# Performance work log

Hardware: AMD Instinct MI355X
Metric: run time of the kernel (lower is better)

Reference implementation:

```python
import jax, jax.numpy as jnp
import numpy as np

N, E = 100000, 1200000
IN_DIM, HID, OUT = 128, 64, 64
EPS = 1e-5


def _glorot(key, shape):
    lim = 1.0 / np.sqrt(shape[0])
    return jax.random.uniform(key, shape, jnp.float32, -lim, lim)


def setup_inputs() -> dict:
    key = jax.random.key(0)
    ks = jax.random.split(key, 20)
    inp = {
        'x': jax.random.normal(ks[0], (N, IN_DIM), jnp.float32),
        'edge_index': jax.random.randint(ks[1], (2, E), 0, N, jnp.int64),
        'xgb_scores': jax.random.uniform(ks[2], (N,), jnp.float32),
        # SAGEConv params: W_l (aggregated path, with bias), W_r (root path, no bias)
        'W1l': _glorot(ks[3], (IN_DIM, HID)), 'b1': jnp.zeros((HID,), jnp.float32), 'W1r': _glorot(ks[4], (IN_DIM, HID)),
        'g1': jnp.ones((HID,), jnp.float32), 'be1': jnp.zeros((HID,), jnp.float32),
        'W2l': _glorot(ks[5], (HID, HID)), 'b2': jnp.zeros((HID,), jnp.float32), 'W2r': _glorot(ks[6], (HID, HID)),
        'g2': jnp.ones((HID,), jnp.float32), 'be2': jnp.zeros((HID,), jnp.float32),
        'W3l': _glorot(ks[7], (HID, OUT)), 'b3': jnp.zeros((OUT,), jnp.float32), 'W3r': _glorot(ks[8], (HID, OUT)),
        'g3': jnp.ones((OUT,), jnp.float32), 'be3': jnp.zeros((OUT,), jnp.float32),
        # fusion MLP: Linear(out+1, 64) -> ReLU -> Linear(64, 1)
        'Wf1': _glorot(ks[9], (OUT + 1, 64)), 'bf1': jnp.zeros((64,), jnp.float32),
        'Wf2': _glorot(ks[10], (64, 1)), 'bf2': jnp.zeros((1,), jnp.float32),
    }
    return inp


def _sage_conv(x, src, dst, Wl, b, Wr, n):
    # mean aggregation of source features at destination nodes (PyG SAGEConv, aggr='mean')
    agg = jax.ops.segment_sum(x[src], dst, num_segments=n)           # (N, d)
    cnt = jax.ops.segment_sum(jnp.ones((src.shape[0],), x.dtype), dst, num_segments=n)
    mean = agg / jnp.clip(cnt, 1.0)[:, None]
    return mean @ Wl + b + x @ Wr


def _bn(h, g, b):
    mu = jnp.mean(h, axis=0)
    var = jnp.var(h, axis=0)  # biased, as in torch BN training normalization
    return (h - mu) * jax.lax.rsqrt(var + EPS) * g + b


def reference(x, edge_index, xgb_scores,
              W1l, b1, W1r, g1, be1,
              W2l, b2, W2r, g2, be2,
              W3l, b3, W3r, g3, be3,
              Wf1, bf1, Wf2, bf2):
    n = x.shape[0]
    src, dst = edge_index[0], edge_index[1]
    # dropout is identity in eval; BN uses batch statistics
    h = jax.nn.relu(_bn(_sage_conv(x, src, dst, W1l, b1, W1r, n), g1, be1))
    h = jax.nn.relu(_bn(_sage_conv(h, src, dst, W2l, b2, W2r, n), g2, be2))
    h = jax.nn.relu(_bn(_sage_conv(h, src, dst, W3l, b3, W3r, n), g3, be3))
    combined = jnp.concatenate([h, xgb_scores[:, None]], axis=1)     # (N, out+1)
    z = jax.nn.relu(combined @ Wf1 + bf1)
    logits = (z @ Wf2 + bf2)[:, 0]
    return logits
```

## Files before the change

### kernel.cpp

```cpp
#include <hip/hip_runtime.h>


typedef __attribute__((ext_vector_type(8))) short bf16x8;
typedef __attribute__((ext_vector_type(4))) float f32x4;

#define ELLS 48

__device__ __forceinline__ ushort f2bf(float f) {
  unsigned u = __float_as_uint(f);
  return (ushort)((u + 0x7fff + ((u >> 16) & 1)) >> 16);
}
__device__ __forceinline__ float bf2f(ushort h) {
  return __uint_as_float((unsigned)h << 16);
}
__device__ __forceinline__ void unpack8(uint4 v, float* f) {
  f[0] = __uint_as_float(v.x << 16);
  f[1] = __uint_as_float(v.x & 0xffff0000u);
  f[2] = __uint_as_float(v.y << 16);
  f[3] = __uint_as_float(v.y & 0xffff0000u);
  f[4] = __uint_as_float(v.z << 16);
  f[5] = __uint_as_float(v.z & 0xffff0000u);
  f[6] = __uint_as_float(v.w << 16);
  f[7] = __uint_as_float(v.w & 0xffff0000u);
}


__device__ __forceinline__ void prep_one(const float* __restrict__ Wl,
                                         const float* __restrict__ Wr,
                                         ushort* __restrict__ Whi,
                                         ushort* __restrict__ Wlo, int din,
                                         int i) {
  int col = i / din, k = i % din;
  float v = (col < 64) ? Wl[(size_t)k * 64 + col]
                       : Wr[(size_t)k * 64 + (col - 64)];
  ushort h = f2bf(v);
  Whi[i] = h;
  Wlo[i] = f2bf(v - bf2f(h));
}

__global__ __launch_bounds__(256) void prep_all(
    const float* __restrict__ W1l, const float* __restrict__ W1r,
    ushort* __restrict__ Whi1, ushort* __restrict__ Wlo1,
    const float* __restrict__ W2l, const float* __restrict__ W2r,
    ushort* __restrict__ Whi2, ushort* __restrict__ Wlo2,
    const float* __restrict__ W3l, const float* __restrict__ W3r,
    ushort* __restrict__ Whi3, ushort* __restrict__ Wlo3,
    int* __restrict__ deg, float* __restrict__ stats,
    ushort* __restrict__ sent, int n, int nbd) {
  int bid = blockIdx.x;
  const int tid = threadIdx.x;
  if (bid < nbd) {
    int i = bid * 256 + tid;
    if (i < n + 4) deg[i] = 0;
    return;
  }
  bid -= nbd;
  if (bid < 64) {
    prep_one(W1l, W1r, Whi1, Wlo1, 128, bid * 256 + tid);
    return;
  }
  bid -= 64;
  if (bid < 32) {
    prep_one(W2l, W2r, Whi2, Wlo2, 64, bid * 256 + tid);
    return;
  }
  bid -= 32;
  if (bid < 32) {
    prep_one(W3l, W3r, Whi3, Wlo3, 64, bid * 256 + tid);
    return;
  }
  if (tid < 384) stats[tid] = 0.f;
  if (tid < 64) sent[tid] = 0;
}


__global__ __launch_bounds__(256) void ell_fill_sharded(
    const int* __restrict__ ei, int* __restrict__ deg, int* __restrict__ ell,
    int E, int n, int bps) {
  const int shard = blockIdx.x / bps;
  const int bib = blockIdx.x % bps;
  const int chunk = n >> 3;
  const int lo = shard * chunk;
  const int hi = (shard == 7) ? n : lo + chunk;
  for (int e = bib * 256 + threadIdx.x; e < E; e += bps * 256) {
    int d = __builtin_nontemporal_load(ei + E + e);
    if (d >= lo && d < hi) {
      int s = __builtin_nontemporal_load(ei + e);
      int pos = atomicAdd(&deg[d], 1);
      if (pos < ELLS) ell[(size_t)d * ELLS + pos] = s;
    }
  }
}

template <int DIN, bool NORM, bool XBF16>
__global__ __launch_bounds__(256) void gemm_mfma(
    const void* __restrict__ Xv, const float* __restrict__ stats,
    const float* __restrict__ g, const float* __restrict__ be,
    const float* __restrict__ bias, const ushort* __restrict__ Whi,
    const ushort* __restrict__ Wlo, ushort* __restrict__ Ybf,
    ushort* __restrict__ Yrbf, int n) {
  constexpr int WS = 40;
  __shared__ ushort sW[2 * 128 * WS];
  __shared__ float sSS[128];
  __shared__ float sB[64];
  const int tid = threadIdx.x;
  const int w = tid >> 6;
  const int lane = tid & 63;
  const int m = lane & 15;
  const int quad = lane >> 4;
  const int row0 = blockIdx.x * 64;

  if (tid < 64) {
    sB[tid] = bias[tid];
    if (NORM) {
      float invn = 1.0f / (float)n;
      float mu = stats[tid] * invn;
      float var = fmaf(-mu, mu, stats[64 + tid] * invn);
      float sc = g[tid] * rsqrtf(var + 1e-5f);
      sSS[tid] = sc;
      sSS[64 + tid] = fmaf(-mu, sc, be[tid]);
    }
  }

  const int arow = min(row0 + w * 16 + m, n - 1);

  f32x4 acc[8];
#pragma unroll
  for (int t = 0; t < 8; t++) acc[t] = (f32x4){0.f, 0.f, 0.f, 0.f};

  for (int kc = 0; kc < DIN; kc += 32) {
    __syncthreads();
    for (int i = tid; i < 512; i += 256) {
      int col = i >> 2;
      int k = (i & 3) * 8;
      *reinterpret_cast<uint4*>(sW + col * WS + k) =
          *reinterpret_cast<const uint4*>(Whi + (size_t)col * DIN + kc + k);
      *reinterpret_cast<uint4*>(sW + 128 * WS + col * WS + k) =
          *reinterpret_cast<const uint4*>(Wlo + (size_t)col * DIN + kc + k);
    }
    __syncthreads();

    const int kb = kc + quad * 8;
    float av[8];
    if (XBF16) {
      const ushort* X = (const ushort*)Xv;
      uint4 v = *reinterpret_cast<const uint4*>(X + (size_t)arow * DIN + kb);
      unpack8(v, av);
    } else {
      const float* X = (const float*)Xv;
      const float* ap = X + (size_t)arow * DIN + kb;
      float4 a0 = *reinterpret_cast<const float4*>(ap);
      float4 a1 = *reinterpret_cast<const float4*>(ap + 4);
      av[0] = a0.x; av[1] = a0.y; av[2] = a0.z; av[3] = a0.w;
      av[4] = a1.x; av[5] = a1.y; av[6] = a1.z; av[7] = a1.w;
    }
    if (NORM) {
#pragma unroll
      for (int j = 0; j < 8; j++)
        av[j] = fmaxf(fmaf(av[j], sSS[kb + j], sSS[64 + kb + j]), 0.f);
    }
    bf16x8 Ahi, Alo;
#pragma unroll
    for (int j = 0; j < 8; j++) {
      ushort h = f2bf(av[j]);
      Ahi[j] = (short)h;
      Alo[j] = (short)f2bf(av[j] - bf2f(h));
    }
#pragma unroll
    for (int t = 0; t < 8; t++) {
      bf16x8 Bhi =
          *reinterpret_cast<const bf16x8*>(sW + (t * 16 + m) * WS + quad * 8);
      bf16x8 Blo = *reinterpret_cast<const bf16x8*>(sW + 128 * WS +
                                                    (t * 16 + m) * WS +
                                                    quad * 8);
      acc[t] = __builtin_amdgcn_mfma_f32_16x16x32_bf16(Ahi, Bhi, acc[t], 0, 0, 0);
      acc[t] = __builtin_amdgcn_mfma_f32_16x16x32_bf16(Ahi, Blo, acc[t], 0, 0, 0);
      acc[t] = __builtin_amdgcn_mfma_f32_16x16x32_bf16(Alo, Bhi, acc[t], 0, 0, 0);
    }
  }

#pragma unroll
  for (int t = 0; t < 8; t++) {
    int col = t * 16 + m;
#pragma unroll
    for (int r = 0; r < 4; r++) {
      int grow = row0 + w * 16 + quad * 4 + r;
      if (grow < n) {
        float v = acc[t][r];
        if (t < 4) {
          Ybf[(size_t)grow * 64 + col] = f2bf(v);
        } else {
          Yrbf[(size_t)grow * 64 + (col - 64)] = f2bf(v + sB[col - 64]);
        }
      }
    }
  }
}

__global__ __launch_bounds__(256) void gather_combine(
    const ushort* __restrict__ Ybf, const ushort* __restrict__ Yrbf,
    const int* __restrict__ ell, const int* __restrict__ deg,
    ushort* __restrict__ Tbf, float* __restrict__ stats, int n) {
  const int lane = threadIdx.x & 63;
  const int w = threadIdx.x >> 6;
  const int grp = lane >> 3;
  const int sub = lane & 7;
  const int wid = blockIdx.x * 4 + w;
  const int nw = gridDim.x * 4;
  float ssum[8], ssq[8];
#pragma unroll
  for (int c = 0; c < 8; c++) ssum[c] = ssq[c] = 0.f;

  for (int base = wid * 4; base < n; base += nw * 4) {
    int4 dg4 = *reinterpret_cast<const int4*>(deg + base);
    int dg[4] = {dg4.x, dg4.y, dg4.z, dg4.w};
    int mx = 0;
#pragma unroll
    for (int j = 0; j < 4; j++) mx = max(mx, min(dg[j], ELLS));
    float a[4][8];
#pragma unroll
    for (int j = 0; j < 4; j++)
#pragma unroll
      for (int c = 0; c < 8; c++) a[j][c] = 0.f;

    for (int e0 = 0; e0 < mx; e0 += 8) {
      int idx = e0 + grp;
      int s0 = ell[(size_t)(base + 0) * ELLS + idx];
      int s1 = ell[(size_t)(base + 1) * ELLS + idx];
      int s2 = ell[(size_t)(base + 2) * ELLS + idx];
      int s3 = ell[(size_t)(base + 3) * ELLS + idx];
      s0 = (idx < dg[0]) ? s0 : n;
      s1 = (idx < dg[1]) ? s1 : n;
      s2 = (idx < dg[2]) ? s2 : n;
      s3 = (idx < dg[3]) ? s3 : n;
      uint4 v0 = *reinterpret_cast<const uint4*>(Ybf + (size_t)s0 * 64 + sub * 8);
      uint4 v1 = *reinterpret_cast<const uint4*>(Ybf + (size_t)s1 * 64 + sub * 8);
      uint4 v2 = *reinterpret_cast<const uint4*>(Ybf + (size_t)s2 * 64 + sub * 8);
      uint4 v3 = *reinterpret_cast<const uint4*>(Ybf + (size_t)s3 * 64 + sub * 8);
      float f[8];
      unpack8(v0, f);
#pragma unroll
      for (int c = 0; c < 8; c++) a[0][c] += f[c];
      unpack8(v1, f);
#pragma unroll
      for (int c = 0; c < 8; c++) a[1][c] += f[c];
      unpack8(v2, f);
#pragma unroll
      for (int c = 0; c < 8; c++) a[2][c] += f[c];
      unpack8(v3, f);
#pragma unroll
      for (int c = 0; c < 8; c++) a[3][c] += f[c];
    }
#pragma unroll
    for (int mmask = 8; mmask <= 32; mmask <<= 1)
#pragma unroll
      for (int j = 0; j < 4; j++)
#pragma unroll
        for (int c = 0; c < 8; c++)
          a[j][c] += __shfl_xor(a[j][c], mmask, 64);

    if (lane < 8) {
#pragma unroll
      for (int j = 0; j < 4; j++) {
        int node = base + j;
        if (node >= n) continue;
        float iv = 1.0f / (float)max(dg[j], 1);
        uint4 yrv =
            *reinterpret_cast<const uint4*>(Yrbf + (size_t)node * 64 + sub * 8);
        float yr[8];
        unpack8(yrv, yr);
        float t[8];
#pragma unroll
        for (int c = 0; c < 8; c++) {
          t[c] = fmaf(a[j][c], iv, yr[c]);
          ssum[c] += t[c];
          ssq[c] = fmaf(t[c], t[c], ssq[c]);
        }
        uint4 o;
        o.x = (uint)f2bf(t[0]) | ((uint)f2bf(t[1]) << 16);
        o.y = (uint)f2bf(t[2]) | ((uint)f2bf(t[3]) << 16);
        o.z = (uint)f2bf(t[4]) | ((uint)f2bf(t[5]) << 16);
        o.w = (uint)f2bf(t[6]) | ((uint)f2bf(t[7]) << 16);
        *reinterpret_cast<uint4*>(Tbf + (size_t)node * 64 + sub * 8) = o;
      }
    }
  }
  __shared__ float rS[4][64];
  __shared__ float rQ[4][64];
  if (lane < 8) {
#pragma unroll
    for (int c = 0; c < 8; c++) {
      rS[w][sub * 8 + c] = ssum[c];
      rQ[w][sub * 8 + c] = ssq[c];
    }
  }
  __syncthreads();
  if (threadIdx.x < 64) {
    int tc = threadIdx.x;
    float s = rS[0][tc] + rS[1][tc] + rS[2][tc] + rS[3][tc];
    float qq = rQ[0][tc] + rQ[1][tc] + rQ[2][tc] + rQ[3][tc];
    atomicAdd(&stats[tc], s);
    atomicAdd(&stats[64 + tc], qq);
  }
}


__global__ __launch_bounds__(256) void fusion_fused(
    const ushort* __restrict__ Tbf, const float* __restrict__ stats,
    const float* __restrict__ g, const float* __restrict__ be,
    const float* __restrict__ xgb, const float* __restrict__ Wf1,
    const float* __restrict__ bf1, const float* __restrict__ Wf2,
    const float* __restrict__ bf2, float* __restrict__ out, int n) {
  __shared__ float sH[64 * 64];
  __shared__ float sW1[65 * 64];
  __shared__ float sW2[64];
  __shared__ float sSS[128];
  const int tid = threadIdx.x;
  const int c = tid & 63;
  const int w = tid >> 6;
  const int row0 = blockIdx.x * 64;
  if (tid < 64) {
    float invn = 1.0f / (float)n;
    float mu = stats[tid] * invn;
    float var = fmaf(-mu, mu, stats[64 + tid] * invn);
    float sc = g[tid] * rsqrtf(var + 1e-5f);
    sSS[tid] = sc;
    sSS[64 + tid] = fmaf(-mu, sc, be[tid]);
  }
  for (int i = tid; i < 65 * 64; i += 256) sW1[i] = Wf1[i];
  if (tid < 64) sW2[tid] = Wf2[tid];
  __syncthreads();
  for (int i = tid; i < 512; i += 256) {
    int r = i >> 3;
    int k = (i & 7) * 8;
    int row = min(row0 + r, n - 1);
    uint4 v = *reinterpret_cast<const uint4*>(Tbf + (size_t)row * 64 + k);
    float f[8];
    unpack8(v, f);
#pragma unroll
    for (int j = 0; j < 8; j++)
      f[j] = fmaxf(fmaf(f[j], sSS[k + j], sSS[64 + k + j]), 0.f);
    *reinterpret_cast<float4*>(sH + r * 64 + k) =
        make_float4(f[0], f[1], f[2], f[3]);
    *reinterpret_cast<float4*>(sH + r * 64 + k + 4) =
        make_float4(f[4], f[5], f[6], f[7]);
  }
  __syncthreads();
  const float b1v = bf1[c];
  const float wx = sW1[64 * 64 + c];
  const float w2v = sW2[c];
  const float b2v = bf2[0];
  float acc[16];
#pragma unroll
  for (int r = 0; r < 16; r++) acc[r] = b1v;
  for (int kk = 0; kk < 64; kk += 4) {
    float4 hv[16];
#pragma unroll
    for (int r = 0; r < 16; r++)
      hv[r] = *reinterpret_cast<const float4*>(sH + (w * 16 + r) * 64 + kk);
    float w0 = sW1[(kk + 0) * 64 + c];
    float w1 = sW1[(kk + 1) * 64 + c];
    float w2 = sW1[(kk + 2) * 64 + c];
    float w3 = sW1[(kk + 3) * 64 + c];
#pragma unroll
    for (int r = 0; r < 16; r++) {
      acc[r] = fmaf(hv[r].x, w0, acc[r]);
      acc[r] = fmaf(hv[r].y, w1, acc[r]);
      acc[r] = fmaf(hv[r].z, w2, acc[r]);
      acc[r] = fmaf(hv[r].w, w3, acc[r]);
    }
  }
#pragma unroll
  for (int r = 0; r < 16; r++) {
    int row = row0 + w * 16 + r;
    float xv = (row < n) ? xgb[row] : 0.f;
    float z = fmaxf(fmaf(xv, wx, acc[r]), 0.f) * w2v;
#pragma unroll
    for (int off = 32; off > 0; off >>= 1) z += __shfl_xor(z, off, 64);
    if (row < n && c == 0) out[row] = z + b2v;
  }
}


extern "C" void kernel_launch(void* const* d_in, const int* in_sizes, int n_in,
                              void* d_out, int out_size, void* d_ws,
                              size_t ws_size, hipStream_t stream) {
  const float* x = (const float*)d_in[0];
  const int* ei = (const int*)d_in[1];
  const float* xgb = (const float*)d_in[2];
  const float* W1l = (const float*)d_in[3];
  const float* b1 = (const float*)d_in[4];
  const float* W1r = (const float*)d_in[5];
  const float* g1 = (const float*)d_in[6];
  const float* be1 = (const float*)d_in[7];
  const float* W2l = (const float*)d_in[8];
  const float* b2 = (const float*)d_in[9];
  const float* W2r = (const float*)d_in[10];
  const float* g2 = (const float*)d_in[11];
  const float* be2 = (const float*)d_in[12];
  const float* W3l = (const float*)d_in[13];
  const float* b3 = (const float*)d_in[14];
  const float* W3r = (const float*)d_in[15];
  const float* g3 = (const float*)d_in[16];
  const float* be3 = (const float*)d_in[17];
  const float* Wf1 = (const float*)d_in[18];
  const float* bf1 = (const float*)d_in[19];
  const float* Wf2 = (const float*)d_in[20];
  const float* bf2 = (const float*)d_in[21];
  float* out = (float*)d_out;

  const int n = in_sizes[2];
  const int E = in_sizes[1] / 2;

  char* w = (char*)d_ws;
  auto alloc = [&](size_t bytes) {
    void* p = (void*)w;
    w += (bytes + 255) & ~(size_t)255;
    return p;
  };
  int* deg = (int*)alloc((size_t)(n + 4) * 4);
  int* ell = (int*)alloc((size_t)(n + 4) * ELLS * 4);
  ushort* Ybf = (ushort*)alloc((size_t)(n + 1) * 64 * 2);
  ushort* Yrbf = (ushort*)alloc((size_t)n * 64 * 2);
  ushort* Tbf = (ushort*)alloc((size_t)n * 64 * 2);
  ushort* Whi1 = (ushort*)alloc(128 * 128 * 2);
  ushort* Wlo1 = (ushort*)alloc(128 * 128 * 2);
  ushort* Whi2 = (ushort*)alloc(128 * 64 * 2);
  ushort* Wlo2 = (ushort*)alloc(128 * 64 * 2);
  ushort* Whi3 = (ushort*)alloc(128 * 64 * 2);
  ushort* Wlo3 = (ushort*)alloc(128 * 64 * 2);
  float* stats = (float*)alloc(3 * 128 * 4);

  const int nbd = (n + 4 + 255) / 256;
  prep_all<<<nbd + 64 + 32 + 32 + 1, 256, 0, stream>>>(
      W1l, W1r, Whi1, Wlo1, W2l, W2r, Whi2, Wlo2, W3l, W3r, Whi3, Wlo3, deg,
      stats, Ybf + (size_t)n * 64, n, nbd);

  const int bps = 2048;
  ell_fill_sharded<<<8 * bps, 256, 0, stream>>>(ei, deg, ell, E, n, bps);

  const int gTile = (n + 63) / 64;
  const int gGath = 2048;

  gemm_mfma<128, false, false><<<gTile, 256, 0, stream>>>(
      x, nullptr, nullptr, nullptr, b1, Whi1, Wlo1, Ybf, Yrbf, n);
  gather_combine<<<gGath, 256, 0, stream>>>(Ybf, Yrbf, ell, deg, Tbf,
                                            stats + 0, n);

  gemm_mfma<64, true, true><<<gTile, 256, 0, stream>>>(
      Tbf, stats + 0, g1, be1, b2, Whi2, Wlo2, Ybf, Yrbf, n);
  gather_combine<<<gGath, 256, 0, stream>>>(Ybf, Yrbf, ell, deg, Tbf,
                                            stats + 128, n);

  gemm_mfma<64, true, true><<<gTile, 256, 0, stream>>>(
      Tbf, stats + 128, g2, be2, b3, Whi3, Wlo3, Ybf, Yrbf, n);
  gather_combine<<<gGath, 256, 0, stream>>>(Ybf, Yrbf, ell, deg, Tbf,
                                            stats + 256, n);

  fusion_fused<<<gTile, 256, 0, stream>>>(Tbf, stats + 256, g3, be3, xgb, Wf1,
                                          bf1, Wf2, bf2, out, n);
}
```

Before: 480.2 us.

## Fuse ELL fill and first-layer GEMM into one interleaved launch

```diff
diff --git a/kernel.cpp b/kernel.cpp
--- a/kernel.cpp
+++ b/kernel.cpp
@@ -74,20 +74,107 @@
 }
 
 
-__global__ __launch_bounds__(256) void ell_fill_sharded(
+__global__ __launch_bounds__(256) void fill_gemm1(
     const int* __restrict__ ei, int* __restrict__ deg, int* __restrict__ ell,
-    int E, int n, int bps) {
-  const int shard = blockIdx.x / bps;
-  const int bib = blockIdx.x % bps;
-  const int chunk = n >> 3;
-  const int lo = shard * chunk;
-  const int hi = (shard == 7) ? n : lo + chunk;
-  for (int e = bib * 256 + threadIdx.x; e < E; e += bps * 256) {
-    int d = __builtin_nontemporal_load(ei + E + e);
-    if (d >= lo && d < hi) {
-      int s = __builtin_nontemporal_load(ei + e);
-      int pos = atomicAdd(&deg[d], 1);
-      if (pos < ELLS) ell[(size_t)d * ELLS + pos] = s;
+    int E, int n, int bps, const float* __restrict__ X,
+    const float* __restrict__ bias, const ushort* __restrict__ Whi,
+    const ushort* __restrict__ Wlo, ushort* __restrict__ Ybf,
+    ushort* __restrict__ Yrbf, int F, int G) {
+  constexpr int WS = 40;
+  __shared__ ushort sW[2 * 128 * WS];
+  __shared__ float sB[64];
+  const int tid = threadIdx.x;
+  const int bid = blockIdx.x;
+  const int tot = F + G;
+  const int gin = (int)(((long long)(bid + 1) * G) / tot);
+  const int gex = (int)(((long long)bid * G) / tot);
+
+  if (gin == gex) {
+    const int fid = bid - gex;
+    const int shard = fid / bps;
+    const int bib = fid & (bps - 1);
+    const int chunk = n >> 3;
+    const int lo = shard * chunk;
+    const int hi = (shard == 7) ? n : lo + chunk;
+    for (int e = bib * 256 + tid; e < E; e += bps * 256) {
+      int d = __builtin_nontemporal_load(ei + E + e);
+      if (d >= lo && d < hi) {
+        int s = __builtin_nontemporal_load(ei + e);
+        int pos = atomicAdd(&deg[d], 1);
+        if (pos < ELLS) ell[(size_t)d * ELLS + pos] = s;
+      }
+    }
+    return;
+  }
+
+  const int tile = gex;
+  const int w = tid >> 6;
+  const int lane = tid & 63;
+  const int m = lane & 15;
+  const int quad = lane >> 4;
+  const int row0 = tile * 64;
+
+  if (tid < 64) sB[tid] = bias[tid];
+
+  const int arow = min(row0 + w * 16 + m, n - 1);
+
+  f32x4 acc[8];
+#pragma unroll
+  for (int t = 0; t < 8; t++) acc[t] = (f32x4){0.f, 0.f, 0.f, 0.f};
+
+  for (int kc = 0; kc < 128; kc += 32) {
+    __syncthreads();
+    for (int i = tid; i < 512; i += 256) {
+      int col = i >> 2;
+      int k = (i & 3) * 8;
+      *reinterpret_cast<uint4*>(sW + col * WS + k) =
+          *reinterpret_cast<const uint4*>(Whi + (size_t)col * 128 + kc + k);
+      *reinterpret_cast<uint4*>(sW + 128 * WS + col * WS + k) =
+          *reinterpret_cast<const uint4*>(Wlo + (size_t)col * 128 + kc + k);
+    }
+    __syncthreads();
+
+    const int kb = kc + quad * 8;
+    float av[8];
+    const float* ap = X + (size_t)arow * 128 + kb;
+    float4 a0 = *reinterpret_cast<const float4*>(ap);
+    float4 a1 = *reinterpret_cast<const float4*>(ap + 4);
+    av[0] = a0.x; av[1] = a0.y; av[2] = a0.z; av[3] = a0.w;
+    av[4] = a1.x; av[5] = a1.y; av[6] = a1.z; av[7] = a1.w;
+    bf16x8 Ahi, Alo;
+#pragma unroll
+    for (int j = 0; j < 8; j++) {
+      ushort h = f2bf(av[j]);
+      Ahi[j] = (short)h;
+      Alo[j] = (short)f2bf(av[j] - bf2f(h));
+    }
+#pragma unroll
+    for (int t = 0; t < 8; t++) {
+      bf16x8 Bhi =
+          *reinterpret_cast<const bf16x8*>(sW + (t * 16 + m) * WS + quad * 8);
+      bf16x8 Blo = *reinterpret_cast<const bf16x8*>(sW + 128 * WS +
+                                                    (t * 16 + m) * WS +
+                                                    quad * 8);
+      acc[t] = __builtin_amdgcn_mfma_f32_16x16x32_bf16(Ahi, Bhi, acc[t], 0, 0, 0);
+      acc[t] = __builtin_amdgcn_mfma_f32_16x16x32_bf16(Ahi, Blo, acc[t], 0, 0, 0);
+      acc[t] = __builtin_amdgcn_mfma_f32_16x16x32_bf16(Alo, Bhi, acc[t], 0, 0, 0);
+    }
+  }
+
+#pragma unroll
+  for (int t = 0; t < 8; t++) {
+    int col = t * 16 + m;
+#pragma unroll
+    for (int r = 0; r < 4; r++) {
+      int grow = row0 + w * 16 + quad * 4 + r;
+      if (grow < n) {
+        float v = acc[t][r];
+        if (t < 4) {
+          Ybf[(size_t)grow * 64 + col] = f2bf(v);
+        } else {
+          Yrbf[(size_t)grow * 64 + (col - 64)] = f2bf(v + sB[col - 64]);
+        }
+      }
     }
   }
 }
@@ -436,14 +523,14 @@
       W1l, W1r, Whi1, Wlo1, W2l, W2r, Whi2, Wlo2, W3l, W3r, Whi3, Wlo3, deg,
       stats, Ybf + (size_t)n * 64, n, nbd);
 
-  const int bps = 2048;
-  ell_fill_sharded<<<8 * bps, 256, 0, stream>>>(ei, deg, ell, E, n, bps);
-
   const int gTile = (n + 63) / 64;
   const int gGath = 2048;
 
-  gemm_mfma<128, false, false><<<gTile, 256, 0, stream>>>(
-      x, nullptr, nullptr, nullptr, b1, Whi1, Wlo1, Ybf, Yrbf, n);
+  const int bps = 2048;
+  const int F = 8 * bps;
+  const int G = gTile;
+  fill_gemm1<<<F + G, 256, 0, stream>>>(ei, deg, ell, E, n, bps, x, b1, Whi1,
+                                        Wlo1, Ybf, Yrbf, F, G);
   gather_combine<<<gGath, 256, 0, stream>>>(Ybf, Yrbf, ell, deg, Tbf,
                                             stats + 0, n);
 
```

New measurement: 483.3 us. Within noise of the previous version (+0.6%).

## Map ELL fill shards to XCDs and vectorize edge loads

Applied to the files above, without the earlier changes.

```diff
diff --git a/kernel.cpp b/kernel.cpp
--- a/kernel.cpp
+++ b/kernel.cpp
@@ -74,18 +74,40 @@
 }
 
 
-__global__ __launch_bounds__(256) void ell_fill_sharded(
+__global__ __launch_bounds__(256) void ell_fill_xcd(
     const int* __restrict__ ei, int* __restrict__ deg, int* __restrict__ ell,
     int E, int n, int bps) {
-  const int shard = blockIdx.x / bps;
-  const int bib = blockIdx.x % bps;
+  const int shard = blockIdx.x & 7;
+  const int bib = blockIdx.x >> 3;
   const int chunk = n >> 3;
   const int lo = shard * chunk;
   const int hi = (shard == 7) ? n : lo + chunk;
-  for (int e = bib * 256 + threadIdx.x; e < E; e += bps * 256) {
-    int d = __builtin_nontemporal_load(ei + E + e);
-    if (d >= lo && d < hi) {
-      int s = __builtin_nontemporal_load(ei + e);
+  const int stride = bps * 256 * 4;
+  const int E4 = E & ~3;
+  for (int e = (bib * 256 + threadIdx.x) * 4; e < E4; e += stride) {
+    int4 d4 = *reinterpret_cast<const int4*>(ei + E + e);
+    int4 s4 = *reinterpret_cast<const int4*>(ei + e);
+    if (d4.x >= lo && d4.x < hi) {
+      int p = atomicAdd(&deg[d4.x], 1);
+      if (p < ELLS) ell[(size_t)d4.x * ELLS + p] = s4.x;
+    }
+    if (d4.y >= lo && d4.y < hi) {
+      int p = atomicAdd(&deg[d4.y], 1);
+      if (p < ELLS) ell[(size_t)d4.y * ELLS + p] = s4.y;
+    }
+    if (d4.z >= lo && d4.z < hi) {
+      int p = atomicAdd(&deg[d4.z], 1);
+      if (p < ELLS) ell[(size_t)d4.z * ELLS + p] = s4.z;
+    }
+    if (d4.w >= lo && d4.w < hi) {
+      int p = atomicAdd(&deg[d4.w], 1);
+      if (p < ELLS) ell[(size_t)d4.w * ELLS + p] = s4.w;
+    }
+  }
+  if (shard == 0 && bib == 0) {
+    for (int e = E4 + threadIdx.x; e < E; e += 256) {
+      int d = ei[E + e];
+      int s = ei[e];
       int pos = atomicAdd(&deg[d], 1);
       if (pos < ELLS) ell[(size_t)d * ELLS + pos] = s;
     }
@@ -436,8 +458,8 @@
       W1l, W1r, Whi1, Wlo1, W2l, W2r, Whi2, Wlo2, W3l, W3r, Whi3, Wlo3, deg,
       stats, Ybf + (size_t)n * 64, n, nbd);
 
-  const int bps = 2048;
-  ell_fill_sharded<<<8 * bps, 256, 0, stream>>>(ei, deg, ell, E, n, bps);
+  const int bps = 128;
+  ell_fill_xcd<<<8 * bps, 256, 0, stream>>>(ei, deg, ell, E, n, bps);
 
   const int gTile = (n + 63) / 64;
   const int gGath = 2048;
```

Result: faster. 469.9 us (-2.2%).

## Fuse all stages into a persistent cooperative megakernel with grid syncs

Applied to the files above, without the earlier changes.

```diff
diff --git a/kernel.cpp b/kernel.cpp
--- a/kernel.cpp
+++ b/kernel.cpp
@@ -1,10 +1,31 @@
 #include <hip/hip_runtime.h>
+#include <hip/hip_cooperative_groups.h>
+
+namespace cg = cooperative_groups;
 
 
 typedef __attribute__((ext_vector_type(8))) short bf16x8;
 typedef __attribute__((ext_vector_type(4))) float f32x4;
 
 #define ELLS 48
+#define SMB 21504
+
+struct MegaArgs {
+  const int* ei;
+  const float* x;
+  const float* xgb;
+  const float *W1l, *b1, *W1r, *g1, *be1;
+  const float *W2l, *b2, *W2r, *g2, *be2;
+  const float *W3l, *b3, *W3r, *g3, *be3;
+  const float *Wf1, *bf1, *Wf2, *bf2;
+  float* out;
+  int* deg;
+  int* ell;
+  ushort *Ybf, *Yrbf, *Tbf;
+  ushort *Whi1, *Wlo1, *Whi2, *Wlo2, *Whi3, *Wlo3;
+  float* stats;
+  int n, E, nblk, F;
+};
 
 __device__ __forceinline__ ushort f2bf(float f) {
   unsigned u = __float_as_uint(f);
@@ -38,77 +59,81 @@
   Wlo[i] = f2bf(v - bf2f(h));
 }
 
-__global__ __launch_bounds__(256) void prep_all(
-    const float* __restrict__ W1l, const float* __restrict__ W1r,
-    ushort* __restrict__ Whi1, ushort* __restrict__ Wlo1,
-    const float* __restrict__ W2l, const float* __restrict__ W2r,
-    ushort* __restrict__ Whi2, ushort* __restrict__ Wlo2,
-    const float* __restrict__ W3l, const float* __restrict__ W3r,
-    ushort* __restrict__ Whi3, ushort* __restrict__ Wlo3,
-    int* __restrict__ deg, float* __restrict__ stats,
-    ushort* __restrict__ sent, int n, int nbd) {
-  int bid = blockIdx.x;
+__device__ __forceinline__ void prep_block(const MegaArgs& a, int vb, int nbd,
+                                           int tid) {
+  if (vb < nbd) {
+    int i = vb * 256 + tid;
+    if (i < a.n + 4) a.deg[i] = 0;
+    return;
+  }
+  vb -= nbd;
+  if (vb < 64) { prep_one(a.W1l, a.W1r, a.Whi1, a.Wlo1, 128, vb * 256 + tid); return; }
+  vb -= 64;
+  if (vb < 32) { prep_one(a.W2l, a.W2r, a.Whi2, a.Wlo2, 64, vb * 256 + tid); return; }
+  vb -= 32;
+  if (vb < 32) { prep_one(a.W3l, a.W3r, a.Whi3, a.Wlo3, 64, vb * 256 + tid); return; }
+  if (tid < 384) a.stats[tid] = 0.f;
+  if (tid < 64) a.Ybf[(size_t)a.n * 64 + tid] = 0;
+}
+
+
+__device__ __forceinline__ void fill_role(const MegaArgs& a, int bid, int bps) {
   const int tid = threadIdx.x;
-  if (bid < nbd) {
-    int i = bid * 256 + tid;
-    if (i < n + 4) deg[i] = 0;
-    return;
-  }
-  bid -= nbd;
-  if (bid < 64) {
-    prep_one(W1l, W1r, Whi1, Wlo1, 128, bid * 256 + tid);
-    return;
-  }
-  bid -= 64;
-  if (bid < 32) {
-    prep_one(W2l, W2r, Whi2, Wlo2, 64, bid * 256 + tid);
-    return;
-  }
-  bid -= 32;
-  if (bid < 32) {
-    prep_one(W3l, W3r, Whi3, Wlo3, 64, bid * 256 + tid);
-    return;
-  }
-  if (tid < 384) stats[tid] = 0.f;
-  if (tid < 64) sent[tid] = 0;
-}
-
-
-__global__ __launch_bounds__(256) void ell_fill_sharded(
-    const int* __restrict__ ei, int* __restrict__ deg, int* __restrict__ ell,
-    int E, int n, int bps) {
-  const int shard = blockIdx.x / bps;
-  const int bib = blockIdx.x % bps;
-  const int chunk = n >> 3;
+  const int shard = bid & 7;
+  const int bib = bid >> 3;
+  const int chunk = a.n >> 3;
   const int lo = shard * chunk;
-  const int hi = (shard == 7) ? n : lo + chunk;
-  for (int e = bib * 256 + threadIdx.x; e < E; e += bps * 256) {
-    int d = __builtin_nontemporal_load(ei + E + e);
-    if (d >= lo && d < hi) {
-      int s = __builtin_nontemporal_load(ei + e);
-      int pos = atomicAdd(&deg[d], 1);
-      if (pos < ELLS) ell[(size_t)d * ELLS + pos] = s;
-    }
-  }
-}
+  const int hi = (shard == 7) ? a.n : lo + chunk;
+  const int stride = bps * 256 * 4;
+  const int E4 = a.E & ~3;
+  for (int e = (bib * 256 + tid) * 4; e < E4; e += stride) {
+    int4 d4 = *reinterpret_cast<const int4*>(a.ei + a.E + e);
+    int4 s4 = *reinterpret_cast<const int4*>(a.ei + e);
+    if (d4.x >= lo && d4.x < hi) {
+      int p = atomicAdd(&a.deg[d4.x], 1);
+      if (p < ELLS) a.ell[(size_t)d4.x * ELLS + p] = s4.x;
+    }
+    if (d4.y >= lo && d4.y < hi) {
+      int p = atomicAdd(&a.deg[d4.y], 1);
+      if (p < ELLS) a.ell[(size_t)d4.y * ELLS + p] = s4.y;
+    }
+    if (d4.z >= lo && d4.z < hi) {
+      int p = atomicAdd(&a.deg[d4.z], 1);
+      if (p < ELLS) a.ell[(size_t)d4.z * ELLS + p] = s4.z;
+    }
+    if (d4.w >= lo && d4.w < hi) {
+      int p = atomicAdd(&a.deg[d4.w], 1);
+      if (p < ELLS) a.ell[(size_t)d4.w * ELLS + p] = s4.w;
+    }
+  }
+  if (bid == 0) {
+    for (int e = E4 + tid; e < a.E; e += 256) {
+      int d = a.ei[a.E + e];
+      int s = a.ei[e];
+      int pos = atomicAdd(&a.deg[d], 1);
+      if (pos < ELLS) a.ell[(size_t)d * ELLS + pos] = s;
+    }
+  }
+}
+
 
 template <int DIN, bool NORM, bool XBF16>
-__global__ __launch_bounds__(256) void gemm_mfma(
+__device__ __forceinline__ void gemm_tile(char* smraw, int tile,
     const void* __restrict__ Xv, const float* __restrict__ stats,
     const float* __restrict__ g, const float* __restrict__ be,
     const float* __restrict__ bias, const ushort* __restrict__ Whi,
     const ushort* __restrict__ Wlo, ushort* __restrict__ Ybf,
     ushort* __restrict__ Yrbf, int n) {
   constexpr int WS = 40;
-  __shared__ ushort sW[2 * 128 * WS];
-  __shared__ float sSS[128];
-  __shared__ float sB[64];
+  ushort* sW = (ushort*)smraw;
+  float* sSS = (float*)(smraw + 20480);
+  float* sB = (float*)(smraw + 20992);
   const int tid = threadIdx.x;
   const int w = tid >> 6;
   const int lane = tid & 63;
   const int m = lane & 15;
   const int quad = lane >> 4;
-  const int row0 = blockIdx.x * 64;
+  const int row0 = tile * 64;
 
   if (tid < 64) {
     sB[tid] = bias[tid];
@@ -171,8 +196,7 @@
       bf16x8 Bhi =
           *reinterpret_cast<const bf16x8*>(sW + (t * 16 + m) * WS + quad * 8);
       bf16x8 Blo = *reinterpret_cast<const bf16x8*>(sW + 128 * WS +
-                                                    (t * 16 + m) * WS +
-                                                    quad * 8);
+                                                    (t * 16 + m) * WS + quad * 8);
       acc[t] = __builtin_amdgcn_mfma_f32_16x16x32_bf16(Ahi, Bhi, acc[t], 0, 0, 0);
       acc[t] = __builtin_amdgcn_mfma_f32_16x16x32_bf16(Ahi, Blo, acc[t], 0, 0, 0);
       acc[t] = __builtin_amdgcn_mfma_f32_16x16x32_bf16(Alo, Bhi, acc[t], 0, 0, 0);
@@ -197,31 +221,36 @@
   }
 }
 
-__global__ __launch_bounds__(256) void gather_combine(
-    const ushort* __restrict__ Ybf, const ushort* __restrict__ Yrbf,
-    const int* __restrict__ ell, const int* __restrict__ deg,
-    ushort* __restrict__ Tbf, float* __restrict__ stats, int n) {
+
+__device__ void gather_stage(char* smraw, const MegaArgs& a,
+                             float* __restrict__ statsL, int bid, int nblk) {
+  float* rS = (float*)smraw;
+  float* rQ = (float*)(smraw + 1024);
   const int lane = threadIdx.x & 63;
   const int w = threadIdx.x >> 6;
   const int grp = lane >> 3;
   const int sub = lane & 7;
-  const int wid = blockIdx.x * 4 + w;
-  const int nw = gridDim.x * 4;
+  const int wid = bid * 4 + w;
+  const int nw = nblk * 4;
+  const int n = a.n;
+  const ushort* __restrict__ Ybf = a.Ybf;
+  const ushort* __restrict__ Yrbf = a.Yrbf;
+  const int* __restrict__ ell = a.ell;
   float ssum[8], ssq[8];
 #pragma unroll
   for (int c = 0; c < 8; c++) ssum[c] = ssq[c] = 0.f;
 
   for (int base = wid * 4; base < n; base += nw * 4) {
-    int4 dg4 = *reinterpret_cast<const int4*>(deg + base);
+    int4 dg4 = *reinterpret_cast<const int4*>(a.deg + base);
     int dg[4] = {dg4.x, dg4.y, dg4.z, dg4.w};
     int mx = 0;
 #pragma unroll
     for (int j = 0; j < 4; j++) mx = max(mx, min(dg[j], ELLS));
-    float a[4][8];
+    float acc[4][8];
 #pragma unroll
     for (int j = 0; j < 4; j++)
 #pragma unroll
-      for (int c = 0; c < 8; c++) a[j][c] = 0.f;
+      for (int c = 0; c < 8; c++) acc[j][c] = 0.f;
 
     for (int e0 = 0; e0 < mx; e0 += 8) {
       int idx = e0 + grp;
@@ -240,16 +269,16 @@
       float f[8];
       unpack8(v0, f);
 #pragma unroll
-      for (int c = 0; c < 8; c++) a[0][c] += f[c];
+      for (int c = 0; c < 8; c++) acc[0][c] += f[c];
       unpack8(v1, f);
 #pragma unroll
-      for (int c = 0; c < 8; c++) a[1][c] += f[c];
+      for (int c = 0; c < 8; c++) acc[1][c] += f[c];
       unpack8(v2, f);
 #pragma unroll
-      for (int c = 0; c < 8; c++) a[2][c] += f[c];
+      for (int c = 0; c < 8; c++) acc[2][c] += f[c];
       unpack8(v3, f);
 #pragma unroll
-      for (int c = 0; c < 8; c++) a[3][c] += f[c];
+      for (int c = 0; c < 8; c++) acc[3][c] += f[c];
     }
 #pragma unroll
     for (int mmask = 8; mmask <= 32; mmask <<= 1)
@@ -257,7 +286,7 @@
       for (int j = 0; j < 4; j++)
 #pragma unroll
         for (int c = 0; c < 8; c++)
-          a[j][c] += __shfl_xor(a[j][c], mmask, 64);
+          acc[j][c] += __shfl_xor(acc[j][c], mmask, 64);
 
     if (lane < 8) {
 #pragma unroll
@@ -272,7 +301,7 @@
         float t[8];
 #pragma unroll
         for (int c = 0; c < 8; c++) {
-          t[c] = fmaf(a[j][c], iv, yr[c]);
+          t[c] = fmaf(acc[j][c], iv, yr[c]);
           ssum[c] += t[c];
           ssq[c] = fmaf(t[c], t[c], ssq[c]);
         }
@@ -281,75 +310,69 @@
         o.y = (uint)f2bf(t[2]) | ((uint)f2bf(t[3]) << 16);
         o.z = (uint)f2bf(t[4]) | ((uint)f2bf(t[5]) << 16);
         o.w = (uint)f2bf(t[6]) | ((uint)f2bf(t[7]) << 16);
-        *reinterpret_cast<uint4*>(Tbf + (size_t)node * 64 + sub * 8) = o;
+        *reinterpret_cast<uint4*>(a.Tbf + (size_t)node * 64 + sub * 8) = o;
       }
     }
   }
-  __shared__ float rS[4][64];
-  __shared__ float rQ[4][64];
+  __syncthreads();
   if (lane < 8) {
 #pragma unroll
     for (int c = 0; c < 8; c++) {
-      rS[w][sub * 8 + c] = ssum[c];
-      rQ[w][sub * 8 + c] = ssq[c];
+      rS[w * 64 + sub * 8 + c] = ssum[c];
+      rQ[w * 64 + sub * 8 + c] = ssq[c];
     }
   }
   __syncthreads();
   if (threadIdx.x < 64) {
     int tc = threadIdx.x;
-    float s = rS[0][tc] + rS[1][tc] + rS[2][tc] + rS[3][tc];
-    float qq = rQ[0][tc] + rQ[1][tc] + rQ[2][tc] + rQ[3][tc];
-    atomicAdd(&stats[tc], s);
-    atomicAdd(&stats[64 + tc], qq);
-  }
-}
-
-
-__global__ __launch_bounds__(256) void fusion_fused(
-    const ushort* __restrict__ Tbf, const float* __restrict__ stats,
-    const float* __restrict__ g, const float* __restrict__ be,
-    const float* __restrict__ xgb, const float* __restrict__ Wf1,
-    const float* __restrict__ bf1, const float* __restrict__ Wf2,
-    const float* __restrict__ bf2, float* __restrict__ out, int n) {
-  __shared__ float sH[64 * 64];
-  __shared__ float sW1[65 * 64];
-  __shared__ float sW2[64];
-  __shared__ float sSS[128];
+    float s = rS[tc] + rS[64 + tc] + rS[128 + tc] + rS[192 + tc];
+    float qq = rQ[tc] + rQ[64 + tc] + rQ[128 + tc] + rQ[192 + tc];
+    atomicAdd(&statsL[tc], s);
+    atomicAdd(&statsL[64 + tc], qq);
+  }
+}
+
+
+__device__ __forceinline__ void fusion_tile(char* smraw, int tile,
+                                            const MegaArgs& a) {
+  float* sH = (float*)smraw;
+  float* fS = (float*)(smraw + 16384);
   const int tid = threadIdx.x;
   const int c = tid & 63;
   const int w = tid >> 6;
-  const int row0 = blockIdx.x * 64;
+  const int row0 = tile * 64;
+  const int n = a.n;
+  const float* stats3 = a.stats + 256;
+  __syncthreads();
   if (tid < 64) {
     float invn = 1.0f / (float)n;
-    float mu = stats[tid] * invn;
-    float var = fmaf(-mu, mu, stats[64 + tid] * invn);
-    float sc = g[tid] * rsqrtf(var + 1e-5f);
-    sSS[tid] = sc;
-    sSS[64 + tid] = fmaf(-mu, sc, be[tid]);
-  }
-  for (int i = tid; i < 65 * 64; i += 256) sW1[i] = Wf1[i];
-  if (tid < 64) sW2[tid] = Wf2[tid];
+    float mu = stats3[tid] * invn;
+    float var = fmaf(-mu, mu, stats3[64 + tid] * invn);
+    float sc = a.g3[tid] * rsqrtf(var + 1e-5f);
+    fS[tid] = sc;
+    fS[64 + tid] = fmaf(-mu, sc, a.be3[tid]);
+  }
   __syncthreads();
   for (int i = tid; i < 512; i += 256) {
     int r = i >> 3;
     int k = (i & 7) * 8;
     int row = min(row0 + r, n - 1);
-    uint4 v = *reinterpret_cast<const uint4*>(Tbf + (size_t)row * 64 + k);
+    uint4 v = *reinterpret_cast<const uint4*>(a.Tbf + (size_t)row * 64 + k);
     float f[8];
     unpack8(v, f);
 #pragma unroll
     for (int j = 0; j < 8; j++)
-      f[j] = fmaxf(fmaf(f[j], sSS[k + j], sSS[64 + k + j]), 0.f);
+      f[j] = fmaxf(fmaf(f[j], fS[k + j], fS[64 + k + j]), 0.f);
     *reinterpret_cast<float4*>(sH + r * 64 + k) =
         make_float4(f[0], f[1], f[2], f[3]);
     *reinterpret_cast<float4*>(sH + r * 64 + k + 4) =
         make_float4(f[4], f[5], f[6], f[7]);
   }
   __syncthreads();
-  const float b1v = bf1[c];
-  const float wx = sW1[64 * 64 + c];
-  const float w2v = sW2[c];
-  const float b2v = bf2[0];
+  const float b1v = a.bf1[c];
+  const float wx = a.Wf1[64 * 64 + c];
+  const float w2v = a.Wf2[c];
+  const float b2v = a.bf2[0];
   float acc[16];
 #pragma unroll
   for (int r = 0; r < 16; r++) acc[r] = b1v;
@@ -358,10 +381,10 @@
 #pragma unroll
     for (int r = 0; r < 16; r++)
       hv[r] = *reinterpret_cast<const float4*>(sH + (w * 16 + r) * 64 + kk);
-    float w0 = sW1[(kk + 0) * 64 + c];
-    float w1 = sW1[(kk + 1) * 64 + c];
-    float w2 = sW1[(kk + 2) * 64 + c];
-    float w3 = sW1[(kk + 3) * 64 + c];
+    float w0 = a.Wf1[(kk + 0) * 64 + c];
+    float w1 = a.Wf1[(kk + 1) * 64 + c];
+    float w2 = a.Wf1[(kk + 2) * 64 + c];
+    float w3 = a.Wf1[(kk + 3) * 64 + c];
 #pragma unroll
     for (int r = 0; r < 16; r++) {
       acc[r] = fmaf(hv[r].x, w0, acc[r]);
@@ -373,12 +396,90 @@
 #pragma unroll
   for (int r = 0; r < 16; r++) {
     int row = row0 + w * 16 + r;
-    float xv = (row < n) ? xgb[row] : 0.f;
+    float xv = (row < n) ? a.xgb[row] : 0.f;
     float z = fmaxf(fmaf(xv, wx, acc[r]), 0.f) * w2v;
 #pragma unroll
     for (int off = 32; off > 0; off >>= 1) z += __shfl_xor(z, off, 64);
-    if (row < n && c == 0) out[row] = z + b2v;
-  }
+    if (row < n && c == 0) a.out[row] = z + b2v;
+  }
+}
+
+
+__global__ __launch_bounds__(256) void mega(MegaArgs a) {
+  __shared__ __align__(16) char sm[SMB];
+  cg::grid_group gg = cg::this_grid();
+  const int bid = blockIdx.x;
+  const int tid = threadIdx.x;
+  const int G = (a.n + 63) / 64;
+  const int nbd = (a.n + 4 + 255) / 256;
+  const int nvb = nbd + 64 + 32 + 32 + 1;
+
+  for (int vb = bid; vb < nvb; vb += a.nblk) prep_block(a, vb, nbd, tid);
+  gg.sync();
+
+  if (bid < a.F) {
+    fill_role(a, bid, a.F >> 3);
+  } else {
+    for (int t = bid - a.F; t < G; t += a.nblk - a.F)
+      gemm_tile<128, false, false>(sm, t, a.x, nullptr, nullptr, nullptr, a.b1,
+                                   a.Whi1, a.Wlo1, a.Ybf, a.Yrbf, a.n);
+  }
+  gg.sync();
+
+  gather_stage(sm, a, a.stats, bid, a.nblk);
+  gg.sync();
+
+  for (int t = bid; t < G; t += a.nblk)
+    gemm_tile<64, true, true>(sm, t, a.Tbf, a.stats, a.g1, a.be1, a.b2, a.Whi2,
+                              a.Wlo2, a.Ybf, a.Yrbf, a.n);
+  gg.sync();
+
+  gather_stage(sm, a, a.stats + 128, bid, a.nblk);
+  gg.sync();
+
+  for (int t = bid; t < G; t += a.nblk)
+    gemm_tile<64, true, true>(sm, t, a.Tbf, a.stats + 128, a.g2, a.be2, a.b3,
+                              a.Whi3, a.Wlo3, a.Ybf, a.Yrbf, a.n);
+  gg.sync();
+
+  gather_stage(sm, a, a.stats + 256, bid, a.nblk);
+  gg.sync();
+
+  for (int t = bid; t < G; t += a.nblk) fusion_tile(sm, t, a);
+}
+
+
+__global__ __launch_bounds__(256) void prep_k(MegaArgs a) {
+  prep_block(a, blockIdx.x, (a.n + 4 + 255) / 256, threadIdx.x);
+}
+__global__ __launch_bounds__(256) void fillgemm1_k(MegaArgs a) {
+  __shared__ __align__(16) char sm[SMB];
+  const int G = (a.n + 63) / 64;
+  if ((int)blockIdx.x < a.F) {
+    fill_role(a, blockIdx.x, a.F >> 3);
+    return;
+  }
+  int t = blockIdx.x - a.F;
+  if (t < G)
+    gemm_tile<128, false, false>(sm, t, a.x, nullptr, nullptr, nullptr, a.b1,
+                                 a.Whi1, a.Wlo1, a.Ybf, a.Yrbf, a.n);
+}
+__global__ __launch_bounds__(256) void gemm_k(MegaArgs a, int layer) {
+  __shared__ __align__(16) char sm[SMB];
+  if (layer == 2)
+    gemm_tile<64, true, true>(sm, blockIdx.x, a.Tbf, a.stats, a.g1, a.be1,
+                              a.b2, a.Whi2, a.Wlo2, a.Ybf, a.Yrbf, a.n);
+  else
+    gemm_tile<64, true, true>(sm, blockIdx.x, a.Tbf, a.stats + 128, a.g2,
+                              a.be2, a.b3, a.Whi3, a.Wlo3, a.Ybf, a.Yrbf, a.n);
+}
+__global__ __launch_bounds__(256) void gather_k(MegaArgs a, int so) {
+  __shared__ __align__(16) char sm2[2048];
+  gather_stage(sm2, a, a.stats + so, blockIdx.x, gridDim.x);
+}
+__global__ __launch_bounds__(256) void fusion_k(MegaArgs a) {
+  __shared__ __align__(16) char sm[SMB];
+  fusion_tile(sm, blockIdx.x, a);
 }
 
 
@@ -388,26 +489,6 @@
   const float* x = (const float*)d_in[0];
   const int* ei = (const int*)d_in[1];
   const float* xgb = (const float*)d_in[2];
-  const float* W1l = (const float*)d_in[3];
-  const float* b1 = (const float*)d_in[4];
-  const float* W1r = (const float*)d_in[5];
-  const float* g1 = (const float*)d_in[6];
-  const float* be1 = (const float*)d_in[7];
-  const float* W2l = (const float*)d_in[8];
-  const float* b2 = (const float*)d_in[9];
-  const float* W2r = (const float*)d_in[10];
-  const float* g2 = (const float*)d_in[11];
-  const float* be2 = (const float*)d_in[12];
-  const float* W3l = (const float*)d_in[13];
-  const float* b3 = (const float*)d_in[14];
-  const float* W3r = (const float*)d_in[15];
-  const float* g3 = (const float*)d_in[16];
-  const float* be3 = (const float*)d_in[17];
-  const float* Wf1 = (const float*)d_in[18];
-  const float* bf1 = (const float*)d_in[19];
-  const float* Wf2 = (const float*)d_in[20];
-  const float* bf2 = (const float*)d_in[21];
-  float* out = (float*)d_out;
 
   const int n = in_sizes[2];
   const int E = in_sizes[1] / 2;
@@ -431,32 +512,66 @@
   ushort* Wlo3 = (ushort*)alloc(128 * 64 * 2);
   float* stats = (float*)alloc(3 * 128 * 4);
 
-  const int nbd = (n + 4 + 255) / 256;
-  prep_all<<<nbd + 64 + 32 + 32 + 1, 256, 0, stream>>>(
-      W1l, W1r, Whi1, Wlo1, W2l, W2r, Whi2, Wlo2, W3l, W3r, Whi3, Wlo3, deg,
-      stats, Ybf + (size_t)n * 64, n, nbd);
-
-  const int bps = 2048;
-  ell_fill_sharded<<<8 * bps, 256, 0, stream>>>(ei, deg, ell, E, n, bps);
-
-  const int gTile = (n + 63) / 64;
-  const int gGath = 2048;
-
-  gemm_mfma<128, false, false><<<gTile, 256, 0, stream>>>(
-      x, nullptr, nullptr, nullptr, b1, Whi1, Wlo1, Ybf, Yrbf, n);
-  gather_combine<<<gGath, 256, 0, stream>>>(Ybf, Yrbf, ell, deg, Tbf,
-                                            stats + 0, n);
-
-  gemm_mfma<64, true, true><<<gTile, 256, 0, stream>>>(
-      Tbf, stats + 0, g1, be1, b2, Whi2, Wlo2, Ybf, Yrbf, n);
-  gather_combine<<<gGath, 256, 0, stream>>>(Ybf, Yrbf, ell, deg, Tbf,
-                                            stats + 128, n);
-
-  gemm_mfma<64, true, true><<<gTile, 256, 0, stream>>>(
-      Tbf, stats + 128, g2, be2, b3, Whi3, Wlo3, Ybf, Yrbf, n);
-  gather_combine<<<gGath, 256, 0, stream>>>(Ybf, Yrbf, ell, deg, Tbf,
-                                            stats + 256, n);
-
-  fusion_fused<<<gTile, 256, 0, stream>>>(Tbf, stats + 256, g3, be3, xgb, Wf1,
-                                          bf1, Wf2, bf2, out, n);
-}
+  MegaArgs ma;
+  ma.ei = ei; ma.x = x; ma.xgb = xgb;
+  ma.W1l = (const float*)d_in[3];  ma.b1 = (const float*)d_in[4];
+  ma.W1r = (const float*)d_in[5];  ma.g1 = (const float*)d_in[6];
+  ma.be1 = (const float*)d_in[7];
+  ma.W2l = (const float*)d_in[8];  ma.b2 = (const float*)d_in[9];
+  ma.W2r = (const float*)d_in[10]; ma.g2 = (const float*)d_in[11];
+  ma.be2 = (const float*)d_in[12];
+  ma.W3l = (const float*)d_in[13]; ma.b3 = (const float*)d_in[14];
+  ma.W3r = (const float*)d_in[15]; ma.g3 = (const float*)d_in[16];
+  ma.be3 = (const float*)d_in[17];
+  ma.Wf1 = (const float*)d_in[18]; ma.bf1 = (const float*)d_in[19];
+  ma.Wf2 = (const float*)d_in[20]; ma.bf2 = (const float*)d_in[21];
+  ma.out = (float*)d_out;
+  ma.deg = deg; ma.ell = ell;
+  ma.Ybf = Ybf; ma.Yrbf = Yrbf; ma.Tbf = Tbf;
+  ma.Whi1 = Whi1; ma.Wlo1 = Wlo1; ma.Whi2 = Whi2; ma.Wlo2 = Wlo2;
+  ma.Whi3 = Whi3; ma.Wlo3 = Wlo3;
+  ma.stats = stats;
+  ma.n = n; ma.E = E;
+
+  static int s_nblk = 0;
+  if (s_nblk == 0) {
+    int perCU = 0;
+    if (hipOccupancyMaxActiveBlocksPerMultiprocessor(
+            &perCU, reinterpret_cast<const void*>(mega), 256, 0) !=
+            hipSuccess ||
+        perCU <= 0)
+      perCU = 4;
+    int ncu = 256;
+    hipDeviceProp_t prop;
+    int dev = 0;
+    (void)hipGetDevice(&dev);
+    if (hipGetDeviceProperties(&prop, dev) == hipSuccess &&
+        prop.multiProcessorCount > 0)
+      ncu = prop.multiProcessorCount;
+    s_nblk = (perCU * ncu) & ~7;
+    if (s_nblk < 256) s_nblk = 256;
+  }
+  ma.nblk = s_nblk;
+  ma.F = ((s_nblk * 2) / 5) & ~7;
+  if (ma.F < 8) ma.F = 8;
+
+  void* kargs[] = {(void*)&ma};
+  hipError_t err = hipLaunchCooperativeKernel(
+      reinterpret_cast<const void*>(mega), dim3(s_nblk), dim3(256), kargs, 0,
+      stream);
+  if (err != hipSuccess) {
+    (void)hipGetLastError();
+    MegaArgs mb = ma;
+    mb.F = 1024;
+    const int G = (n + 63) / 64;
+    const int nbd = (n + 4 + 255) / 256;
+    prep_k<<<nbd + 129, 256, 0, stream>>>(mb);
+    fillgemm1_k<<<mb.F + G, 256, 0, stream>>>(mb);
+    gather_k<<<2048, 256, 0, stream>>>(mb, 0);
+    gemm_k<<<G, 256, 0, stream>>>(mb, 2);
+    gather_k<<<2048, 256, 0, stream>>>(mb, 128);
+    gemm_k<<<G, 256, 0, stream>>>(mb, 3);
+    gather_k<<<2048, 256, 0, stream>>>(mb, 256);
+    fusion_k<<<G, 256, 0, stream>>>(mb);
+  }
+}
```

Result: slower. 1.053 ms (+119.2%).
